# Optimization experiments

Measured on AMD Instinct MI355X. Metric: run time of the kernel, lower is better.

The kernel has to match this reference:

```python
import jax, jax.numpy as jnp
import numpy as np

B = 1_000_000   # batched RHS evaluation points
T = 1461        # days of forcing data (~4 years)
H = 16          # hidden width of ET_net / Q_net


def _step(x):
    # step_fct from models.common_net: smooth Heaviside
    return (jnp.tanh(5.0 * x) + 1.0) * 0.5


def _mlp(x, w1, b1, w2, b2, w3, b3):
    h = jnp.tanh(x @ w1 + b1)
    h = jnp.tanh(h @ w2 + b2)
    return (h @ w3 + b3)[:, 0]


def setup_inputs() -> dict:
    key = jax.random.key(0)
    ks = jax.random.split(key, 12)
    inp = {}
    inp["t"] = jax.random.uniform(ks[0], (B,), jnp.float32) * (T - 1)
    # S[:,0]=S_snow, S[:,1]=S_water  (storages in mm)
    inp["S"] = jax.random.uniform(ks[1], (B, 2), jnp.float32) * 500.0
    inp["ts"] = jnp.arange(T, dtype=jnp.float32)
    inp["precp_series"] = jax.random.uniform(ks[2], (T,), jnp.float32) * 20.0
    inp["temp_series"] = jax.random.uniform(ks[3], (T,), jnp.float32) * 30.0 - 10.0
    inp["lday_series"] = jax.random.uniform(ks[4], (T,), jnp.float32) * 0.2 + 0.3

    def lin(k, i, o):
        return jax.random.normal(k, (i, o), jnp.float32) * (1.0 / np.sqrt(i))

    inp["et_w1"] = lin(ks[5], 3, H); inp["et_b1"] = jnp.zeros((H,), jnp.float32)
    inp["et_w2"] = lin(ks[6], H, H); inp["et_b2"] = jnp.zeros((H,), jnp.float32)
    inp["et_w3"] = lin(ks[7], H, 1); inp["et_b3"] = jnp.zeros((1,), jnp.float32)
    inp["q_w1"] = lin(ks[8], 2, H); inp["q_b1"] = jnp.zeros((H,), jnp.float32)
    inp["q_w2"] = lin(ks[9], H, H); inp["q_b2"] = jnp.zeros((H,), jnp.float32)
    inp["q_w3"] = lin(ks[10], H, 1); inp["q_b3"] = jnp.zeros((1,), jnp.float32)
    # physics params: f, Smax, Qmax, Df, Tmax, Tmin
    inp["f"] = jnp.float32(0.5)
    inp["Smax"] = jnp.float32(1000.0)
    inp["Qmax"] = jnp.float32(20.0)
    inp["Df"] = jnp.float32(2.0)
    inp["Tmax"] = jnp.float32(1.0)
    inp["Tmin"] = jnp.float32(-1.0)
    return inp


def reference(t, S, ts, precp_series, temp_series, lday_series,
              et_w1, et_b1, et_w2, et_b2, et_w3, et_b3,
              q_w1, q_b1, q_w2, q_b2, q_w3, q_b3,
              f, Smax, Qmax, Df, Tmax, Tmin):
    # clamp_parameters()
    f = jnp.clip(f, 0.0, 1.0)
    Smax = jnp.clip(Smax, 100.0, 1500.0)
    Qmax = jnp.clip(Qmax, 10.0, 50.0)
    Df = jnp.clip(Df, 0.01, 5.0)
    Tmax = jnp.clip(Tmax, 0.0, 3.0)
    Tmin = jnp.clip(Tmin, -3.0, 0.0)

    # forcing interpolation (interp.evaluate(t))
    precp = jnp.interp(t, ts, precp_series)
    temp = jnp.interp(t, ts, temp_series)
    lday = jnp.interp(t, ts, lday_series)

    S_snow, S_water = S[:, 0], S[:, 1]

    ET = _mlp(jnp.stack([S_snow, S_water, temp], axis=-1),
              et_w1, et_b1, et_w2, et_b2, et_w3, et_b3)  # [B]
    Q = _mlp(jnp.stack([S_water, precp], axis=-1),
             q_w1, q_b1, q_w2, q_b2, q_w3, q_b3)          # [B]

    # M: snowmelt
    melt = _step(temp - Tmax) * _step(S_snow) * jnp.minimum(S_snow, Df * (temp - Tmax))
    # Ps / Pr: snow / rain partition of precipitation
    dS_1 = _step(Tmin - temp) * precp - melt
    dS_2 = (_step(temp - Tmin) * precp + melt
            - _step(S_water) * lday * jnp.exp(ET)
            - _step(S_water) * jnp.exp(Q))
    return jnp.stack([dS_1, dS_2], axis=-1)  # [B, 2]
```

## Files before the change

### kernel.cpp

```cpp
#include <hip/hip_runtime.h>

#define TLEN 1461
#define L2E      1.44269504088896340736f
#define TWO_L2E  2.88539008177792681472f

typedef __bf16 bf16x8 __attribute__((ext_vector_type(8)));
typedef float f32x16 __attribute__((ext_vector_type(16)));

union FragU { unsigned u[4]; bf16x8 f; };

__device__ __forceinline__ float step_fn(float x) {
    float e = __builtin_amdgcn_exp2f(x * -14.4269504088896341f);
    return __builtin_amdgcn_rcpf(1.0f + e);
}
__device__ __forceinline__ unsigned cvt_pk_bf16(float lo, float hi) {
    unsigned r;
    asm("v_cvt_pk_bf16_f32 %0, %1, %2" : "=v"(r) : "v"(lo), "v"(hi));
    return r;
}
__device__ __forceinline__ void plswap(unsigned &a, unsigned &b) {
    asm("v_permlane32_swap_b32 %0, %1" : "+v"(a), "+v"(b));
}
__device__ __forceinline__ float plswap_add(float a, float b) {
    unsigned ua = __float_as_uint(a), ub = __float_as_uint(b);
    plswap(ua, ub);
    return __uint_as_float(ua) + __uint_as_float(ub);
}

__device__ __forceinline__ void quad_tanh_pack(float y0, float y1, float y2, float y3,
                                               unsigned &wlo, unsigned &whi) {
    float s0 = __builtin_amdgcn_rcpf(1.0f + __builtin_amdgcn_exp2f(y0));
    float s1 = __builtin_amdgcn_rcpf(1.0f + __builtin_amdgcn_exp2f(y1));
    float s2 = __builtin_amdgcn_rcpf(1.0f + __builtin_amdgcn_exp2f(y2));
    float s3 = __builtin_amdgcn_rcpf(1.0f + __builtin_amdgcn_exp2f(y3));
    float h0 = fmaf(-2.0f, s0, 1.0f), h1 = fmaf(-2.0f, s1, 1.0f);
    float h2 = fmaf(-2.0f, s2, 1.0f), h3 = fmaf(-2.0f, s3, 1.0f);
    wlo = cvt_pk_bf16(h0, h1);
    whi = cvt_pk_bf16(h2, h3);
}

template <int BASE>
__device__ __forceinline__ float tail_slim(const FragU a2,
    const float* __restrict__ b2, const float* __restrict__ w3,
    float pinit, bool hi, const FragU ba, const FragU bb)
{
    f32x16 c0, c1;
#pragma unroll
    for (int r = 0; r < 8; ++r) {
        const int j0 = (r & 3) + 8 * (r >> 2);
        float jb = TWO_L2E * (hi ? b2[j0 + 4] : b2[j0]);
        c0[BASE + r] = jb;
        c1[BASE + r] = jb;
    }
    c0 = __builtin_amdgcn_mfma_f32_32x32x16_bf16(a2.f, ba.f, c0, 0, 0, 0);
    c1 = __builtin_amdgcn_mfma_f32_32x32x16_bf16(a2.f, bb.f, c1, 0, 0, 0);

    float p0 = pinit, p1 = pinit;
#pragma unroll
    for (int r = 0; r < 8; ++r) {
        const int j0 = (r & 3) + 8 * (r >> 2);
        float w3n = -TWO_L2E * (hi ? w3[j0 + 4] : w3[j0]);
        float s0 = __builtin_amdgcn_rcpf(1.0f + __builtin_amdgcn_exp2f(c0[BASE + r]));
        float s1 = __builtin_amdgcn_rcpf(1.0f + __builtin_amdgcn_exp2f(c1[BASE + r]));
        p0 = fmaf(w3n, s0, p0);
        p1 = fmaf(w3n, s1, p1);
    }
    return plswap_add(p0, p1);
}

__device__ __forceinline__ float2 sample_pipeline(
    float tv, float S_snow, float S_water,
    const float4* __restrict__ s_tbl, const FragU a2,
    float pinit_e, float pinit_q, bool hi,
    float Df, float Tmax, float Tmin,
    const float* __restrict__ g_ew1, const float* __restrict__ g_eb1,
    const float* __restrict__ g_eb2, const float* __restrict__ g_ew3,
    const float* __restrict__ g_qw1, const float* __restrict__ g_qb1,
    const float* __restrict__ g_qb2, const float* __restrict__ g_qw3)
{
    int idx = (int)tv;
    idx = max(0, min(idx, TLEN - 2));
    const float fr = tv - (float)idx;
    const float4 t0 = s_tbl[idx];
    const float4 t1 = s_tbl[idx + 1];
    const float precp = fmaf(fr, t1.x - t0.x, t0.x);
    const float temp  = fmaf(fr, t1.y - t0.y, t0.y);
    const float lday  = fmaf(fr, t1.z - t0.z, t0.z);

    unsigned elo[4], ehi[4], qlo[4], qhi[4];
#pragma unroll
    for (int j4 = 0; j4 < 4; ++j4) {
        float4 b4 = *reinterpret_cast<const float4*>(&g_eb1[j4 * 4]);
        float4 w0 = *reinterpret_cast<const float4*>(&g_ew1[0 * 16 + j4 * 4]);
        float4 w1 = *reinterpret_cast<const float4*>(&g_ew1[1 * 16 + j4 * 4]);
        float4 w2 = *reinterpret_cast<const float4*>(&g_ew1[2 * 16 + j4 * 4]);
        float y0 = TWO_L2E * fmaf(temp, w2.x, fmaf(S_water, w1.x, fmaf(S_snow, w0.x, b4.x)));
        float y1 = TWO_L2E * fmaf(temp, w2.y, fmaf(S_water, w1.y, fmaf(S_snow, w0.y, b4.y)));
        float y2 = TWO_L2E * fmaf(temp, w2.z, fmaf(S_water, w1.z, fmaf(S_snow, w0.z, b4.z)));
        float y3 = TWO_L2E * fmaf(temp, w2.w, fmaf(S_water, w1.w, fmaf(S_snow, w0.w, b4.w)));
        unsigned wl, wh;
        quad_tanh_pack(y0, y1, y2, y3, wl, wh);
        if (j4 < 2) { elo[j4 * 2] = wl; elo[j4 * 2 + 1] = wh; }
        else        { ehi[(j4 - 2) * 2] = wl; ehi[(j4 - 2) * 2 + 1] = wh; }
    }
#pragma unroll
    for (int j4 = 0; j4 < 4; ++j4) {
        float4 b4 = *reinterpret_cast<const float4*>(&g_qb1[j4 * 4]);
        float4 w0 = *reinterpret_cast<const float4*>(&g_qw1[0 * 16 + j4 * 4]);
        float4 w1 = *reinterpret_cast<const float4*>(&g_qw1[1 * 16 + j4 * 4]);
        float y0 = TWO_L2E * fmaf(precp, w1.x, fmaf(S_water, w0.x, b4.x));
        float y1 = TWO_L2E * fmaf(precp, w1.y, fmaf(S_water, w0.y, b4.y));
        float y2 = TWO_L2E * fmaf(precp, w1.z, fmaf(S_water, w0.z, b4.z));
        float y3 = TWO_L2E * fmaf(precp, w1.w, fmaf(S_water, w0.w, b4.w));
        unsigned wl, wh;
        quad_tanh_pack(y0, y1, y2, y3, wl, wh);
        if (j4 < 2) { qlo[j4 * 2] = wl; qlo[j4 * 2 + 1] = wh; }
        else        { qhi[(j4 - 2) * 2] = wl; qhi[(j4 - 2) * 2 + 1] = wh; }
    }

    FragU bae, bbe, baq, bbq;
#pragma unroll
    for (int p = 0; p < 4; ++p) {
        unsigned l = elo[p], h = ehi[p];
        plswap(l, h);
        bae.u[p] = l; bbe.u[p] = h;
        l = qlo[p]; h = qhi[p];
        plswap(l, h);
        baq.u[p] = l; bbq.u[p] = h;
    }

    const float ETs = tail_slim<0>(a2, g_eb2, g_ew3, pinit_e, hi, bae, bbe);
    const float Qs  = tail_slim<8>(a2, g_qb2, g_qw3, pinit_q, hi, baq, bbq);

    const float sw_step = step_fn(S_water);
    const float sp      = step_fn(temp - Tmin);
    const float melt = step_fn(temp - Tmax) * step_fn(S_snow)
                     * fminf(S_snow, Df * (temp - Tmax));
    const float dS1 = (1.0f - sp) * precp - melt;
    const float dS2 = sp * precp + melt
                    - sw_step * fmaf(lday, __builtin_amdgcn_exp2f(ETs),
                                     __builtin_amdgcn_exp2f(Qs));
    return make_float2(dS1, dS2);
}

__global__ __launch_bounds__(256, 4) void hydro_kernel(
    const float* __restrict__ g_t,
    const float* __restrict__ g_S,
    const float* __restrict__ g_precp,
    const float* __restrict__ g_temp,
    const float* __restrict__ g_lday,
    const float* __restrict__ g_ew1, const float* __restrict__ g_eb1,
    const float* __restrict__ g_ew2, const float* __restrict__ g_eb2,
    const float* __restrict__ g_ew3, const float* __restrict__ g_eb3,
    const float* __restrict__ g_qw1, const float* __restrict__ g_qb1,
    const float* __restrict__ g_qw2, const float* __restrict__ g_qb2,
    const float* __restrict__ g_qw3, const float* __restrict__ g_qb3,
    const float* __restrict__ g_Df, const float* __restrict__ g_Tmax,
    const float* __restrict__ g_Tmin,
    float* __restrict__ g_out, int B)
{
    __shared__ __align__(16) float4 s_tbl[TLEN];

    const int tx = threadIdx.x;
    for (int i = tx; i < TLEN; i += 256) {
        s_tbl[i] = make_float4(g_precp[i], g_temp[i], g_lday[i], 0.0f);
    }
    __syncthreads();

    const int lane = tx & 63;
    const int m  = lane & 31;
    const bool hi = (lane >> 5) != 0;

    FragU a2;
    {
        const float* wsrc = (m < 16) ? g_ew2 : g_qw2;
        const int mm = m & 15;
        const int kg8 = hi ? 8 : 0;
#pragma unroll
        for (int p = 0; p < 4; ++p) {
            const int k0 = kg8 + 2 * p, k1 = k0 + 1;
            a2.u[p] = cvt_pk_bf16(TWO_L2E * wsrc[k0 * 16 + mm],
                                  TWO_L2E * wsrc[k1 * 16 + mm]);
        }
    }

    float slo_e = 0.0f, shi_e = 0.0f, slo_q = 0.0f, shi_q = 0.0f;
#pragma unroll
    for (int r = 0; r < 8; ++r) {
        const int j0 = (r & 3) + 8 * (r >> 2);
        slo_e += g_ew3[j0]; shi_e += g_ew3[j0 + 4];
        slo_q += g_qw3[j0]; shi_q += g_qw3[j0 + 4];
    }
    const float pinit_e = L2E * fmaf(0.5f, g_eb3[0], hi ? shi_e : slo_e);
    const float pinit_q = L2E * fmaf(0.5f, g_qb3[0], hi ? shi_q : slo_q);

    const float Df   = fminf(fmaxf(g_Df[0],   0.01f), 5.0f);
    const float Tmax = fminf(fmaxf(g_Tmax[0], 0.0f),  3.0f);
    const float Tmin = fminf(fmaxf(g_Tmin[0], -3.0f), 0.0f);

    const int i0 = blockIdx.x * 512 + tx;
    const int i1 = i0 + 256;
    const int c0i = (i0 < B) ? i0 : (B - 1);
    const int c1i = (i1 < B) ? i1 : (B - 1);

    const float tv0 = g_t[c0i];
    const float tv1 = g_t[c1i];
    const float2 Sv0 = reinterpret_cast<const float2*>(g_S)[c0i];
    const float2 Sv1 = reinterpret_cast<const float2*>(g_S)[c1i];

    const float2 r0 = sample_pipeline(tv0, Sv0.x, Sv0.y, s_tbl, a2,
                                      pinit_e, pinit_q, hi, Df, Tmax, Tmin,
                                      g_ew1, g_eb1, g_eb2, g_ew3,
                                      g_qw1, g_qb1, g_qb2, g_qw3);
    const float2 r1 = sample_pipeline(tv1, Sv1.x, Sv1.y, s_tbl, a2,
                                      pinit_e, pinit_q, hi, Df, Tmax, Tmin,
                                      g_ew1, g_eb1, g_eb2, g_ew3,
                                      g_qw1, g_qb1, g_qb2, g_qw3);

    if (i0 < B) reinterpret_cast<float2*>(g_out)[i0] = r0;
    if (i1 < B) reinterpret_cast<float2*>(g_out)[i1] = r1;
}

extern "C" void kernel_launch(void* const* d_in, const int* in_sizes, int n_in,
                              void* d_out, int out_size, void* d_ws, size_t ws_size,
                              hipStream_t stream)
{
    const int B = in_sizes[0];
    const int block = 256;
    const int grid = (B + 511) / 512;
    hipLaunchKernelGGL(hydro_kernel, dim3(grid), dim3(block), 0, stream,
        (const float*)d_in[0],
        (const float*)d_in[1],
        (const float*)d_in[3],
        (const float*)d_in[4],
        (const float*)d_in[5],
        (const float*)d_in[6],  (const float*)d_in[7],
        (const float*)d_in[8],  (const float*)d_in[9],
        (const float*)d_in[10], (const float*)d_in[11],
        (const float*)d_in[12], (const float*)d_in[13],
        (const float*)d_in[14], (const float*)d_in[15],
        (const float*)d_in[16], (const float*)d_in[17],
        (const float*)d_in[21],
        (const float*)d_in[22],
        (const float*)d_in[23],
        (float*)d_out, B);
}
```

Measured before the change: 26.61 us.

## Process one sample per thread with sequential MFMA tails to raise occupancy

Each thread now handles one sample instead of two, and the two layer-2 MFMAs are run one after the other instead of being held in flight together. This lowers register pressure so launch bounds can ask for 8 waves per SIMD instead of 4. The forcing table is split into a float2 (precp, temp) array plus a separate lday array, cutting LDS from 16 to 12 bytes per entry. In exchange, every block reloads the whole table for half as many samples, the setup per thread is paid twice as often, and there is less instruction-level parallelism inside each thread.

```diff
diff --git a/kernel.cpp b/kernel.cpp
--- a/kernel.cpp
+++ b/kernel.cpp
@@ -26,124 +26,53 @@
     plswap(ua, ub);
     return __uint_as_float(ua) + __uint_as_float(ub);
 }
-
-__device__ __forceinline__ void quad_tanh_pack(float y0, float y1, float y2, float y3,
-                                               unsigned &wlo, unsigned &whi) {
-    float s0 = __builtin_amdgcn_rcpf(1.0f + __builtin_amdgcn_exp2f(y0));
-    float s1 = __builtin_amdgcn_rcpf(1.0f + __builtin_amdgcn_exp2f(y1));
-    float s2 = __builtin_amdgcn_rcpf(1.0f + __builtin_amdgcn_exp2f(y2));
-    float s3 = __builtin_amdgcn_rcpf(1.0f + __builtin_amdgcn_exp2f(y3));
-    float h0 = fmaf(-2.0f, s0, 1.0f), h1 = fmaf(-2.0f, s1, 1.0f);
-    float h2 = fmaf(-2.0f, s2, 1.0f), h3 = fmaf(-2.0f, s3, 1.0f);
-    wlo = cvt_pk_bf16(h0, h1);
-    whi = cvt_pk_bf16(h2, h3);
+__device__ __forceinline__ float tanh_pre(float y) {
+    float s = __builtin_amdgcn_rcpf(1.0f + __builtin_amdgcn_exp2f(y));
+    return fmaf(-2.0f, s, 1.0f);
 }
 
 template <int BASE>
-__device__ __forceinline__ float tail_slim(const FragU a2,
+__device__ __forceinline__ float tail_seq(const FragU a2,
     const float* __restrict__ b2, const float* __restrict__ w3,
     float pinit, bool hi, const FragU ba, const FragU bb)
 {
-    f32x16 c0, c1;
-#pragma unroll
-    for (int r = 0; r < 8; ++r) {
-        const int j0 = (r & 3) + 8 * (r >> 2);
-        float jb = TWO_L2E * (hi ? b2[j0 + 4] : b2[j0]);
-        c0[BASE + r] = jb;
-        c1[BASE + r] = jb;
-    }
-    c0 = __builtin_amdgcn_mfma_f32_32x32x16_bf16(a2.f, ba.f, c0, 0, 0, 0);
-    c1 = __builtin_amdgcn_mfma_f32_32x32x16_bf16(a2.f, bb.f, c1, 0, 0, 0);
-
     float p0 = pinit, p1 = pinit;
-#pragma unroll
-    for (int r = 0; r < 8; ++r) {
-        const int j0 = (r & 3) + 8 * (r >> 2);
-        float w3n = -TWO_L2E * (hi ? w3[j0 + 4] : w3[j0]);
-        float s0 = __builtin_amdgcn_rcpf(1.0f + __builtin_amdgcn_exp2f(c0[BASE + r]));
-        float s1 = __builtin_amdgcn_rcpf(1.0f + __builtin_amdgcn_exp2f(c1[BASE + r]));
-        p0 = fmaf(w3n, s0, p0);
-        p1 = fmaf(w3n, s1, p1);
+    {
+        f32x16 c;
+#pragma unroll
+        for (int r = 0; r < 8; ++r) {
+            const int j0 = (r & 3) + 8 * (r >> 2);
+            c[BASE + r] = TWO_L2E * (hi ? b2[j0 + 4] : b2[j0]);
+        }
+        c = __builtin_amdgcn_mfma_f32_32x32x16_bf16(a2.f, ba.f, c, 0, 0, 0);
+#pragma unroll
+        for (int r = 0; r < 8; ++r) {
+            const int j0 = (r & 3) + 8 * (r >> 2);
+            float w3n = -2.0f * L2E * (hi ? w3[j0 + 4] : w3[j0]);
+            float s = __builtin_amdgcn_rcpf(1.0f + __builtin_amdgcn_exp2f(c[BASE + r]));
+            p0 = fmaf(w3n, s, p0);
+        }
+    }
+    {
+        f32x16 c;
+#pragma unroll
+        for (int r = 0; r < 8; ++r) {
+            const int j0 = (r & 3) + 8 * (r >> 2);
+            c[BASE + r] = TWO_L2E * (hi ? b2[j0 + 4] : b2[j0]);
+        }
+        c = __builtin_amdgcn_mfma_f32_32x32x16_bf16(a2.f, bb.f, c, 0, 0, 0);
+#pragma unroll
+        for (int r = 0; r < 8; ++r) {
+            const int j0 = (r & 3) + 8 * (r >> 2);
+            float w3n = -2.0f * L2E * (hi ? w3[j0 + 4] : w3[j0]);
+            float s = __builtin_amdgcn_rcpf(1.0f + __builtin_amdgcn_exp2f(c[BASE + r]));
+            p1 = fmaf(w3n, s, p1);
+        }
     }
     return plswap_add(p0, p1);
 }
 
-__device__ __forceinline__ float2 sample_pipeline(
-    float tv, float S_snow, float S_water,
-    const float4* __restrict__ s_tbl, const FragU a2,
-    float pinit_e, float pinit_q, bool hi,
-    float Df, float Tmax, float Tmin,
-    const float* __restrict__ g_ew1, const float* __restrict__ g_eb1,
-    const float* __restrict__ g_eb2, const float* __restrict__ g_ew3,
-    const float* __restrict__ g_qw1, const float* __restrict__ g_qb1,
-    const float* __restrict__ g_qb2, const float* __restrict__ g_qw3)
-{
-    int idx = (int)tv;
-    idx = max(0, min(idx, TLEN - 2));
-    const float fr = tv - (float)idx;
-    const float4 t0 = s_tbl[idx];
-    const float4 t1 = s_tbl[idx + 1];
-    const float precp = fmaf(fr, t1.x - t0.x, t0.x);
-    const float temp  = fmaf(fr, t1.y - t0.y, t0.y);
-    const float lday  = fmaf(fr, t1.z - t0.z, t0.z);
-
-    unsigned elo[4], ehi[4], qlo[4], qhi[4];
-#pragma unroll
-    for (int j4 = 0; j4 < 4; ++j4) {
-        float4 b4 = *reinterpret_cast<const float4*>(&g_eb1[j4 * 4]);
-        float4 w0 = *reinterpret_cast<const float4*>(&g_ew1[0 * 16 + j4 * 4]);
-        float4 w1 = *reinterpret_cast<const float4*>(&g_ew1[1 * 16 + j4 * 4]);
-        float4 w2 = *reinterpret_cast<const float4*>(&g_ew1[2 * 16 + j4 * 4]);
-        float y0 = TWO_L2E * fmaf(temp, w2.x, fmaf(S_water, w1.x, fmaf(S_snow, w0.x, b4.x)));
-        float y1 = TWO_L2E * fmaf(temp, w2.y, fmaf(S_water, w1.y, fmaf(S_snow, w0.y, b4.y)));
-        float y2 = TWO_L2E * fmaf(temp, w2.z, fmaf(S_water, w1.z, fmaf(S_snow, w0.z, b4.z)));
-        float y3 = TWO_L2E * fmaf(temp, w2.w, fmaf(S_water, w1.w, fmaf(S_snow, w0.w, b4.w)));
-        unsigned wl, wh;
-        quad_tanh_pack(y0, y1, y2, y3, wl, wh);
-        if (j4 < 2) { elo[j4 * 2] = wl; elo[j4 * 2 + 1] = wh; }
-        else        { ehi[(j4 - 2) * 2] = wl; ehi[(j4 - 2) * 2 + 1] = wh; }
-    }
-#pragma unroll
-    for (int j4 = 0; j4 < 4; ++j4) {
-        float4 b4 = *reinterpret_cast<const float4*>(&g_qb1[j4 * 4]);
-        float4 w0 = *reinterpret_cast<const float4*>(&g_qw1[0 * 16 + j4 * 4]);
-        float4 w1 = *reinterpret_cast<const float4*>(&g_qw1[1 * 16 + j4 * 4]);
-        float y0 = TWO_L2E * fmaf(precp, w1.x, fmaf(S_water, w0.x, b4.x));
-        float y1 = TWO_L2E * fmaf(precp, w1.y, fmaf(S_water, w0.y, b4.y));
-        float y2 = TWO_L2E * fmaf(precp, w1.z, fmaf(S_water, w0.z, b4.z));
-        float y3 = TWO_L2E * fmaf(precp, w1.w, fmaf(S_water, w0.w, b4.w));
-        unsigned wl, wh;
-        quad_tanh_pack(y0, y1, y2, y3, wl, wh);
-        if (j4 < 2) { qlo[j4 * 2] = wl; qlo[j4 * 2 + 1] = wh; }
-        else        { qhi[(j4 - 2) * 2] = wl; qhi[(j4 - 2) * 2 + 1] = wh; }
-    }
-
-    FragU bae, bbe, baq, bbq;
-#pragma unroll
-    for (int p = 0; p < 4; ++p) {
-        unsigned l = elo[p], h = ehi[p];
-        plswap(l, h);
-        bae.u[p] = l; bbe.u[p] = h;
-        l = qlo[p]; h = qhi[p];
-        plswap(l, h);
-        baq.u[p] = l; bbq.u[p] = h;
-    }
-
-    const float ETs = tail_slim<0>(a2, g_eb2, g_ew3, pinit_e, hi, bae, bbe);
-    const float Qs  = tail_slim<8>(a2, g_qb2, g_qw3, pinit_q, hi, baq, bbq);
-
-    const float sw_step = step_fn(S_water);
-    const float sp      = step_fn(temp - Tmin);
-    const float melt = step_fn(temp - Tmax) * step_fn(S_snow)
-                     * fminf(S_snow, Df * (temp - Tmax));
-    const float dS1 = (1.0f - sp) * precp - melt;
-    const float dS2 = sp * precp + melt
-                    - sw_step * fmaf(lday, __builtin_amdgcn_exp2f(ETs),
-                                     __builtin_amdgcn_exp2f(Qs));
-    return make_float2(dS1, dS2);
-}
-
-__global__ __launch_bounds__(256, 4) void hydro_kernel(
+__global__ __launch_bounds__(256, 8) void hydro_kernel(
     const float* __restrict__ g_t,
     const float* __restrict__ g_S,
     const float* __restrict__ g_precp,
@@ -159,11 +88,13 @@
     const float* __restrict__ g_Tmin,
     float* __restrict__ g_out, int B)
 {
-    __shared__ __align__(16) float4 s_tbl[TLEN];
+    __shared__ __align__(16) float2 s_pt[TLEN];
+    __shared__ __align__(16) float  s_ld[TLEN];
 
     const int tx = threadIdx.x;
     for (int i = tx; i < TLEN; i += 256) {
-        s_tbl[i] = make_float4(g_precp[i], g_temp[i], g_lday[i], 0.0f);
+        s_pt[i] = make_float2(g_precp[i], g_temp[i]);
+        s_ld[i] = g_lday[i];
     }
     __syncthreads();
 
@@ -198,27 +129,85 @@
     const float Tmax = fminf(fmaxf(g_Tmax[0], 0.0f),  3.0f);
     const float Tmin = fminf(fmaxf(g_Tmin[0], -3.0f), 0.0f);
 
-    const int i0 = blockIdx.x * 512 + tx;
-    const int i1 = i0 + 256;
-    const int c0i = (i0 < B) ? i0 : (B - 1);
-    const int c1i = (i1 < B) ? i1 : (B - 1);
-
-    const float tv0 = g_t[c0i];
-    const float tv1 = g_t[c1i];
-    const float2 Sv0 = reinterpret_cast<const float2*>(g_S)[c0i];
-    const float2 Sv1 = reinterpret_cast<const float2*>(g_S)[c1i];
-
-    const float2 r0 = sample_pipeline(tv0, Sv0.x, Sv0.y, s_tbl, a2,
-                                      pinit_e, pinit_q, hi, Df, Tmax, Tmin,
-                                      g_ew1, g_eb1, g_eb2, g_ew3,
-                                      g_qw1, g_qb1, g_qb2, g_qw3);
-    const float2 r1 = sample_pipeline(tv1, Sv1.x, Sv1.y, s_tbl, a2,
-                                      pinit_e, pinit_q, hi, Df, Tmax, Tmin,
-                                      g_ew1, g_eb1, g_eb2, g_ew3,
-                                      g_qw1, g_qb1, g_qb2, g_qw3);
-
-    if (i0 < B) reinterpret_cast<float2*>(g_out)[i0] = r0;
-    if (i1 < B) reinterpret_cast<float2*>(g_out)[i1] = r1;
+    const int i = blockIdx.x * 256 + tx;
+    const int ic = (i < B) ? i : (B - 1);
+
+    const float tv = g_t[ic];
+    const float2 Sv = reinterpret_cast<const float2*>(g_S)[ic];
+    const float S_snow = Sv.x, S_water = Sv.y;
+
+    int idx = (int)tv;
+    idx = max(0, min(idx, TLEN - 2));
+    const float fr = tv - (float)idx;
+    const float2 pt0 = s_pt[idx];
+    const float2 pt1 = s_pt[idx + 1];
+    const float precp = fmaf(fr, pt1.x - pt0.x, pt0.x);
+    const float temp  = fmaf(fr, pt1.y - pt0.y, pt0.y);
+    const float lday  = fmaf(fr, s_ld[idx + 1] - s_ld[idx], s_ld[idx]);
+
+    float ETs;
+    {
+        unsigned w[8];
+#pragma unroll
+        for (int j4 = 0; j4 < 4; ++j4) {
+            float4 b4 = *reinterpret_cast<const float4*>(&g_eb1[j4 * 4]);
+            float4 w0 = *reinterpret_cast<const float4*>(&g_ew1[0 * 16 + j4 * 4]);
+            float4 w1 = *reinterpret_cast<const float4*>(&g_ew1[1 * 16 + j4 * 4]);
+            float4 w2 = *reinterpret_cast<const float4*>(&g_ew1[2 * 16 + j4 * 4]);
+            float h0 = tanh_pre(TWO_L2E * fmaf(temp, w2.x, fmaf(S_water, w1.x, fmaf(S_snow, w0.x, b4.x))));
+            float h1 = tanh_pre(TWO_L2E * fmaf(temp, w2.y, fmaf(S_water, w1.y, fmaf(S_snow, w0.y, b4.y))));
+            float h2 = tanh_pre(TWO_L2E * fmaf(temp, w2.z, fmaf(S_water, w1.z, fmaf(S_snow, w0.z, b4.z))));
+            float h3 = tanh_pre(TWO_L2E * fmaf(temp, w2.w, fmaf(S_water, w1.w, fmaf(S_snow, w0.w, b4.w))));
+            w[2 * j4]     = cvt_pk_bf16(h0, h1);
+            w[2 * j4 + 1] = cvt_pk_bf16(h2, h3);
+        }
+        FragU ba, bb;
+#pragma unroll
+        for (int p = 0; p < 4; ++p) {
+            unsigned a = w[p], b = w[p + 4];
+            plswap(a, b);
+            ba.u[p] = a; bb.u[p] = b;
+        }
+        ETs = tail_seq<0>(a2, g_eb2, g_ew3, pinit_e, hi, ba, bb);
+    }
+
+    float Qs;
+    {
+        unsigned w[8];
+#pragma unroll
+        for (int j4 = 0; j4 < 4; ++j4) {
+            float4 b4 = *reinterpret_cast<const float4*>(&g_qb1[j4 * 4]);
+            float4 w0 = *reinterpret_cast<const float4*>(&g_qw1[0 * 16 + j4 * 4]);
+            float4 w1 = *reinterpret_cast<const float4*>(&g_qw1[1 * 16 + j4 * 4]);
+            float h0 = tanh_pre(TWO_L2E * fmaf(precp, w1.x, fmaf(S_water, w0.x, b4.x)));
+            float h1 = tanh_pre(TWO_L2E * fmaf(precp, w1.y, fmaf(S_water, w0.y, b4.y)));
+            float h2 = tanh_pre(TWO_L2E * fmaf(precp, w1.z, fmaf(S_water, w0.z, b4.z)));
+            float h3 = tanh_pre(TWO_L2E * fmaf(precp, w1.w, fmaf(S_water, w0.w, b4.w)));
+            w[2 * j4]     = cvt_pk_bf16(h0, h1);
+            w[2 * j4 + 1] = cvt_pk_bf16(h2, h3);
+        }
+        FragU ba, bb;
+#pragma unroll
+        for (int p = 0; p < 4; ++p) {
+            unsigned a = w[p], b = w[p + 4];
+            plswap(a, b);
+            ba.u[p] = a; bb.u[p] = b;
+        }
+        Qs = tail_seq<8>(a2, g_qb2, g_qw3, pinit_q, hi, ba, bb);
+    }
+
+    const float sw_step = step_fn(S_water);
+    const float sp      = step_fn(temp - Tmin);
+    const float melt = step_fn(temp - Tmax) * step_fn(S_snow)
+                     * fminf(S_snow, Df * (temp - Tmax));
+    const float dS1 = (1.0f - sp) * precp - melt;
+    const float dS2 = sp * precp + melt
+                    - sw_step * fmaf(lday, __builtin_amdgcn_exp2f(ETs),
+                                     __builtin_amdgcn_exp2f(Qs));
+
+    if (i < B) {
+        reinterpret_cast<float2*>(g_out)[i] = make_float2(dS1, dS2);
+    }
 }
 
 extern "C" void kernel_launch(void* const* d_in, const int* in_sizes, int n_in,
@@ -227,7 +216,7 @@
 {
     const int B = in_sizes[0];
     const int block = 256;
-    const int grid = (B + 511) / 512;
+    const int grid = (B + block - 1) / block;
     hipLaunchKernelGGL(hydro_kernel, dim3(grid), dim3(block), 0, stream,
         (const float*)d_in[0],
         (const float*)d_in[1],
```

Measured after the change: 27.83 us. 1.05x slower.
